# Optimization experiments

Measured on AMD Instinct MI355X. Metric: run time of the kernel, lower is better.

The kernel has to match this reference:

```python
import jax, jax.numpy as jnp
import numpy as np

L = 4096
E = 512   # embed dim
S = 1024  # state dim
H = 150   # Scorer hidden dim
GI = 2 * S + E
MAX_N = 10


def _scorer(x, W1, b1, W2, b2, W3, b3):
    h = jax.nn.relu(x @ W1 + b1)
    h = jax.nn.relu(h @ W2 + b2)
    return h @ W3 + b3  # [..., 1]


def setup_inputs() -> dict:
    key = jax.random.key(0)
    ks = jax.random.split(key, 16)
    def init(k, shape, fan_in):
        return jax.random.normal(k, shape, dtype=jnp.float32) / np.sqrt(fan_in)
    inp = {
        "embeds": jax.random.normal(ks[0], (L, E), dtype=jnp.float32),
        "states": jax.random.normal(ks[1], (L, S), dtype=jnp.float32),
        # attention Scorer params (input S)
        "aW1": init(ks[2], (S, H), S), "ab1": jnp.zeros((H,), jnp.float32),
        "aW2": init(ks[3], (H, H), H), "ab2": jnp.zeros((H,), jnp.float32),
        "aW3": init(ks[4], (H, 1), H), "ab3": jnp.zeros((1,), jnp.float32),
        # sm Scorer params (input GI)
        "sW1": init(ks[5], (GI, H), GI), "sb1": jnp.zeros((H,), jnp.float32),
        "sW2": init(ks[6], (H, H), H), "sb2": jnp.zeros((H,), jnp.float32),
        "sW3": init(ks[7], (H, 1), H), "sb3": jnp.zeros((1,), jnp.float32),
    }
    return inp


def reference(embeds, states, aW1, ab1, aW2, ab2, aW3, ab3,
              sW1, sb1, sW2, sb2, sW3, sb3):
    # per-token attention logits, computed once: [L]
    attns = _scorer(states, aW1, ab1, aW2, ab2, aW3, ab3)[:, 0]

    gs = []
    for n in range(1, MAX_N + 1):  # fixed small loop over window sizes
        M = L - n + 1                                  # number of windows
        starts = jnp.arange(M)
        idx = starts[:, None] + jnp.arange(n)          # [M, n] token indices
        w = jax.nn.softmax(attns[idx], axis=1)         # windowed softmax [M, n]
        pooled = jnp.einsum('mn,mne->me', w, embeds[idx])  # [M, E]
        g = jnp.concatenate([states[starts], states[starts + n - 1], pooled],
                            axis=1)                    # [M, 2S+E]
        gs.append(g)
    x = jnp.concatenate(gs, axis=0)                    # [T, GI], T = 10L-45
    scores = _scorer(x, sW1, sb1, sW2, sb2, sW3, sb3)[:, 0]  # [T]
    return scores
```

## Files before the change

kernel.cpp:

```cpp
#include <hip/hip_runtime.h>
#include <hip/hip_bf16.h>
#include <math.h>

#define LTOK 4096
#define EDIM 512
#define SDIM 1024
#define HDIM 150
#define PPAD 152
#define MAXN 10
#define TOTAL_ROWS 40915
#define KA 1536
#define NC 640
#define K2 160
#define NKT (KA / 32)

typedef _Float16 hfrag __attribute__((ext_vector_type(8)));
typedef float ffrag __attribute__((ext_vector_type(4)));


#define ITEMS_A   (LTOK * (KA / 8))
#define ITEMS_W   (NC * (KA / 8))
#define ITEMS_W2  (K2 * (K2 / 8))
#define ITEMS_A2  (K2 * (K2 / 8))
#define ITEMS_Z   (LTOK * K2 / 8)
#define ITEMS_TOT (ITEMS_A + ITEMS_W + ITEMS_W2 + ITEMS_A2 + ITEMS_Z)

__global__ __launch_bounds__(256) void prep_kernel(
    const float* __restrict__ embeds, const float* __restrict__ states,
    const float* __restrict__ aW1, const float* __restrict__ aW2,
    const float* __restrict__ sW1, const float* __restrict__ sW2,
    _Float16* __restrict__ Apk, _Float16* __restrict__ Wpk,
    _Float16* __restrict__ W2pk, _Float16* __restrict__ A2pk,
    _Float16* __restrict__ AH1h)
{
    int it = blockIdx.x * 256 + threadIdx.x;
    if (it < ITEMS_A) {
        const int rem = it % 3072;
        const int g = it / 3072, kt = rem >> 6, lane = rem & 63;
        const int row = g * 16 + (lane & 15);
        const int k0 = kt * 32 + (lane >> 4) * 8;
        const float* src = (k0 < SDIM) ? (states + (size_t)row * SDIM + k0)
                                       : (embeds + (size_t)row * EDIM + (k0 - SDIM));
        const float4 v0 = *(const float4*)src;
        const float4 v1 = *(const float4*)(src + 4);
        _Float16 o[8] = {(_Float16)v0.x, (_Float16)v0.y, (_Float16)v0.z, (_Float16)v0.w,
                         (_Float16)v1.x, (_Float16)v1.y, (_Float16)v1.z, (_Float16)v1.w};
        *(uint4*)(Apk + (size_t)it * 8) = *(uint4*)o;
        return;
    }
    it -= ITEMS_A;
    if (it < ITEMS_W) {
        const int rem = it % 3072;
        const int cg = it / 3072, kt = rem >> 6, lane = rem & 63;
        const int col = cg * 16 + (lane & 15);
        const int k0 = kt * 32 + (lane >> 4) * 8;
        const int g4 = (col < 600) ? (col / HDIM) : -1;
        const int cj = col % HDIM;
        _Float16 o[8];
        for (int j = 0; j < 8; ++j) {
            const int k = k0 + j;
            float wv = 0.f;
            if (g4 == 0 && k < SDIM) wv = sW1[(size_t)k * HDIM + cj];
            else if (g4 == 1 && k < SDIM) wv = sW1[(size_t)(SDIM + k) * HDIM + cj];
            else if (g4 == 2 && k < SDIM) wv = aW1[(size_t)k * HDIM + cj];
            else if (g4 == 3 && k >= SDIM) wv = sW1[(size_t)(SDIM + k) * HDIM + cj];
            o[j] = (_Float16)wv;
        }
        const size_t tk = (size_t)cg * 48 + kt;
        *(uint4*)(Wpk + (tk * 64 + lane) * 8) = *(uint4*)o;
        return;
    }
    it -= ITEMS_W;
    if (it < ITEMS_W2 + ITEMS_A2) {
        const bool is_a = (it >= ITEMS_W2);
        const int li = is_a ? (it - ITEMS_W2) : it;
        const float* src = is_a ? aW2 : sW2;
        _Float16* dst = is_a ? A2pk : W2pk;
        const int tk = li >> 6, lane = li & 63;
        const int col = (tk / 5) * 16 + (lane & 15);
        const int k0 = (tk % 5) * 32 + (lane >> 4) * 8;
        _Float16 o[8];
        for (int j = 0; j < 8; ++j) {
            const int k = k0 + j;
            float wv = (col < HDIM && k < HDIM) ? src[(size_t)k * HDIM + col] : 0.f;
            o[j] = (_Float16)wv;
        }
        *(uint4*)(dst + ((size_t)tk * 64 + lane) * 8) = *(uint4*)o;
        return;
    }
    it -= ITEMS_W2 + ITEMS_A2;
    if (it < ITEMS_Z) {
        const uint4 z = {0u, 0u, 0u, 0u};
        *(uint4*)(AH1h + (size_t)it * 8) = z;
    }
}

__global__ __launch_bounds__(256) void k_proj(
    const _Float16* __restrict__ Apk, const _Float16* __restrict__ Wpk,
    const float* __restrict__ ab1,
    float* __restrict__ P1, float* __restrict__ P2,
    float* __restrict__ PE, _Float16* __restrict__ AH1h)
{
    const int bM = blockIdx.x & 63, bN = blockIdx.x >> 6;
    const int tid = threadIdx.x;
    const int w = tid >> 6, lane = tid & 63;
    const int quad = lane >> 4, l16 = lane & 15;
    const int wm = w & 1, wn = w >> 1;

    const int gbase = bM * 4 + wm * 2;
    const int cgbase = bN * 4 + wn * 2;

    ffrag acc[2][2];
#pragma unroll
    for (int t = 0; t < 2; ++t)
#pragma unroll
        for (int u = 0; u < 2; ++u) acc[t][u] = (ffrag){0.f, 0.f, 0.f, 0.f};

    const _Float16* a0p = Apk + ((size_t)(gbase + 0) * NKT) * 512 + lane * 8;
    const _Float16* a1p = Apk + ((size_t)(gbase + 1) * NKT) * 512 + lane * 8;
    const _Float16* b0p = Wpk + ((size_t)(cgbase + 0) * NKT) * 512 + lane * 8;
    const _Float16* b1p = Wpk + ((size_t)(cgbase + 1) * NKT) * 512 + lane * 8;

#pragma unroll 4
    for (int kt = 0; kt < NKT; ++kt) {
        const hfrag a0 = *(const hfrag*)(a0p + (size_t)kt * 512);
        const hfrag a1 = *(const hfrag*)(a1p + (size_t)kt * 512);
        const hfrag b0 = *(const hfrag*)(b0p + (size_t)kt * 512);
        const hfrag b1 = *(const hfrag*)(b1p + (size_t)kt * 512);
        acc[0][0] = __builtin_amdgcn_mfma_f32_16x16x32_f16(a0, b0, acc[0][0], 0, 0, 0);
        acc[1][0] = __builtin_amdgcn_mfma_f32_16x16x32_f16(a1, b0, acc[1][0], 0, 0, 0);
        acc[0][1] = __builtin_amdgcn_mfma_f32_16x16x32_f16(a0, b1, acc[0][1], 0, 0, 0);
        acc[1][1] = __builtin_amdgcn_mfma_f32_16x16x32_f16(a1, b1, acc[1][1], 0, 0, 0);
    }

#pragma unroll
    for (int t = 0; t < 2; ++t)
#pragma unroll
        for (int u = 0; u < 2; ++u) {
            const int col = (cgbase + u) * 16 + l16;
#pragma unroll
            for (int r = 0; r < 4; ++r) {
                const int row = (gbase + t) * 16 + quad * 4 + r;
                const float v = acc[t][u][r];
                if (col < 150)      P1[(size_t)row * PPAD + col] = v;
                else if (col < 300) P2[(size_t)row * PPAD + (col - 150)] = v;
                else if (col < 450) AH1h[(size_t)row * K2 + (col - 300)] =
                                        (_Float16)fmaxf(v + ab1[col - 300], 0.f);
                else if (col < 600) PE[(size_t)row * PPAD + (col - 450)] = v;
            }
        }
}

__global__ __launch_bounds__(64) void attn_tail(
    const _Float16* __restrict__ AH1h, const _Float16* __restrict__ A2pk,
    const float* __restrict__ ab2, const float* __restrict__ aW3,
    const float* __restrict__ ab3, float* __restrict__ attns)
{
    const int tok0 = blockIdx.x * 16;
    const int lane = threadIdx.x;
    const int quad = lane >> 4, l16 = lane & 15;

    hfrag af[5];
#pragma unroll
    for (int ks = 0; ks < 5; ++ks)
        af[ks] = *(const hfrag*)(AH1h + (size_t)(tok0 + l16) * K2 + ks * 32 + quad * 8);

    float part[4] = {0.f, 0.f, 0.f, 0.f};
    for (int ct = 0; ct < 10; ++ct) {
        ffrag acc = (ffrag){0.f, 0.f, 0.f, 0.f};
#pragma unroll
        for (int ks = 0; ks < 5; ++ks) {
            const size_t tk = (size_t)ct * 5 + ks;
            const hfrag fb = *(const hfrag*)(A2pk + (tk * 64 + lane) * 8);
            acc = __builtin_amdgcn_mfma_f32_16x16x32_f16(af[ks], fb, acc, 0, 0, 0);
        }
        const int col = ct * 16 + l16;
        const float s2 = (col < HDIM) ? ab2[col] : 0.f;
        const float s3 = (col < HDIM) ? aW3[col] : 0.f;
#pragma unroll
        for (int r = 0; r < 4; ++r) part[r] += fmaxf(acc[r] + s2, 0.f) * s3;
    }

#pragma unroll
    for (int off = 1; off < 16; off <<= 1) {
#pragma unroll
        for (int r = 0; r < 4; ++r) part[r] += __shfl_xor(part[r], off, 64);
    }
    if (l16 == 0) {
        const float b3 = ab3[0];
#pragma unroll
        for (int r = 0; r < 4; ++r)
            attns[tok0 + quad * 4 + r] = part[r] + b3;
    }
}

#define RB2 64
__global__ __launch_bounds__(256) void span_kernel(
    const float* __restrict__ attns, const float* __restrict__ P1,
    const float* __restrict__ P2, const float* __restrict__ PE,
    const float* __restrict__ sb1, const _Float16* __restrict__ W2pk,
    const float* __restrict__ sb2, const float* __restrict__ sW3,
    const float* __restrict__ sb3, float* __restrict__ out)
{
    const int nIdx = blockIdx.x >> 6, mChunk = blockIdx.x & 63;
    const int n = nIdx + 1;
    const int Mn = LTOK - n + 1;
    const int m0 = mChunk * 64;
    const int nrows = min(64, Mn - m0);
    const int offn = nIdx * LTOK - (nIdx * (nIdx - 1)) / 2;

    const int tid = threadIdx.x;
    const int w = tid >> 6, lane = tid & 63, quad = lane >> 4, l16 = lane & 15;

    __shared__ __align__(16) _Float16 h1h[RB2 * K2];
    __shared__ float wgt[RB2][MAXN];

    if (tid < RB2) {
        const int m = min(m0 + tid, Mn - 1);
        float mx = -1e30f;
        for (int j = 0; j < n; ++j) mx = fmaxf(mx, attns[m + j]);
        float tp[MAXN]; float s = 0.f;
        for (int j = 0; j < n; ++j) { tp[j] = expf(attns[m + j] - mx); s += tp[j]; }
        const float inv = 1.f / s;
#pragma unroll
        for (int j = 0; j < MAXN; ++j) wgt[tid][j] = (j < n) ? tp[j] * inv : 0.f;
    }
    __syncthreads();

    for (int item = tid; item < RB2 * (K2 / 4); item += 256) {
        const int r = item / (K2 / 4), cq = item % (K2 / 4);
        const int c0 = cq * 4;
        const int m = min(m0 + r, Mn - 1);
        float4 a = {0.f, 0.f, 0.f, 0.f};
        if (c0 < HDIM) {
            const float4 p1 = *(const float4*)(P1 + (size_t)m * PPAD + c0);
            const float4 p2 = *(const float4*)(P2 + (size_t)(m + n - 1) * PPAD + c0);
            a.x = p1.x + p2.x; a.y = p1.y + p2.y;
            a.z = p1.z + p2.z; a.w = p1.w + p2.w;
#pragma unroll
            for (int j = 0; j < MAXN; ++j) {
                const int mj = min(m + j, LTOK - 1);
                const float4 pe = *(const float4*)(PE + (size_t)mj * PPAD + c0);
                const float wj = wgt[r][j];
                a.x = fmaf(wj, pe.x, a.x); a.y = fmaf(wj, pe.y, a.y);
                a.z = fmaf(wj, pe.z, a.z); a.w = fmaf(wj, pe.w, a.w);
            }
        }
        _Float16 o[4];
        o[0] = (c0 + 0 < HDIM) ? (_Float16)fmaxf(a.x + sb1[c0 + 0], 0.f) : (_Float16)0.f;
        o[1] = (c0 + 1 < HDIM) ? (_Float16)fmaxf(a.y + sb1[c0 + 1], 0.f) : (_Float16)0.f;
        o[2] = (c0 + 2 < HDIM) ? (_Float16)fmaxf(a.z + sb1[c0 + 2], 0.f) : (_Float16)0.f;
        o[3] = (c0 + 3 < HDIM) ? (_Float16)fmaxf(a.w + sb1[c0 + 3], 0.f) : (_Float16)0.f;
        *(uint2*)&h1h[r * K2 + c0] = *(uint2*)o;
    }
    __syncthreads();

    hfrag af[5];
#pragma unroll
    for (int ks = 0; ks < 5; ++ks)
        af[ks] = *(const hfrag*)&h1h[(w * 16 + l16) * K2 + ks * 32 + quad * 8];

    float part[4] = {0.f, 0.f, 0.f, 0.f};
    for (int ct = 0; ct < 10; ++ct) {
        ffrag acc = (ffrag){0.f, 0.f, 0.f, 0.f};
#pragma unroll
        for (int ks = 0; ks < 5; ++ks) {
            const size_t tk = (size_t)ct * 5 + ks;
            const hfrag fb = *(const hfrag*)(W2pk + (tk * 64 + lane) * 8);
            acc = __builtin_amdgcn_mfma_f32_16x16x32_f16(af[ks], fb, acc, 0, 0, 0);
        }
        const int col = ct * 16 + l16;
        const float s2 = (col < HDIM) ? sb2[col] : 0.f;
        const float s3 = (col < HDIM) ? sW3[col] : 0.f;
#pragma unroll
        for (int r = 0; r < 4; ++r) part[r] += fmaxf(acc[r] + s2, 0.f) * s3;
    }

#pragma unroll
    for (int off = 1; off < 16; off <<= 1) {
#pragma unroll
        for (int r = 0; r < 4; ++r) part[r] += __shfl_xor(part[r], off, 64);
    }
    if (l16 == 0) {
        const float b3 = sb3[0];
#pragma unroll
        for (int r = 0; r < 4; ++r) {
            const int lr = w * 16 + quad * 4 + r;
            if (lr < nrows) out[offn + m0 + lr] = part[r] + b3;
        }
    }
}

extern "C" void kernel_launch(void* const* d_in, const int* in_sizes, int n_in,
                              void* d_out, int out_size, void* d_ws, size_t ws_size,
                              hipStream_t stream) {
    const float* embeds = (const float*)d_in[0];
    const float* states = (const float*)d_in[1];
    const float* aW1 = (const float*)d_in[2];
    const float* ab1 = (const float*)d_in[3];
    const float* aW2 = (const float*)d_in[4];
    const float* ab2 = (const float*)d_in[5];
    const float* aW3 = (const float*)d_in[6];
    const float* ab3 = (const float*)d_in[7];
    const float* sW1 = (const float*)d_in[8];
    const float* sb1 = (const float*)d_in[9];
    const float* sW2 = (const float*)d_in[10];
    const float* sb2 = (const float*)d_in[11];
    const float* sW3 = (const float*)d_in[12];
    const float* sb3 = (const float*)d_in[13];
    float* out = (float*)d_out;

    float* attns = (float*)d_ws;
    float* P1 = attns + LTOK;
    float* P2 = P1 + (size_t)LTOK * PPAD;
    float* PE = P2 + (size_t)LTOK * PPAD;
    _Float16* AH1h = (_Float16*)(PE + (size_t)LTOK * PPAD);
    _Float16* Apk  = AH1h + (size_t)LTOK * K2;
    _Float16* Wpk  = Apk + (size_t)ITEMS_A * 8;
    _Float16* W2pk = Wpk + (size_t)NC * KA;
    _Float16* A2pk = W2pk + (size_t)K2 * K2;

    prep_kernel<<<(ITEMS_TOT + 255) / 256, 256, 0, stream>>>(
        embeds, states, aW1, aW2, sW1, sW2, Apk, Wpk, W2pk, A2pk, AH1h);
    k_proj<<<640, 256, 0, stream>>>(
        Apk, Wpk, ab1, P1, P2, PE, AH1h);
    attn_tail<<<LTOK / 16, 64, 0, stream>>>(
        AH1h, A2pk, ab2, aW3, ab3, attns);
    span_kernel<<<640, 256, 0, stream>>>(
        attns, P1, P2, PE, sb1, W2pk, sb2, sW3, sb3, out);
}
```

Before: 159.6 us.

## Fuse four kernels into one persistent kernel with grid-wide barriers

Merges the prep, projection GEMM, attention tail and span scorer kernels into a single persistent kernel sized to occupancy, separated by atomic-counter grid barriers. The goal is to remove three launch gaps and their tail drain. The attention tail now splits its column tiles across four waves and reduces partial sums in shared memory. The cost is a memset launch, barrier spin overhead, lower occupancy from launch bounds of three blocks, and a deadlock risk if not all blocks are co-resident.

```diff
diff --git a/kernel.cpp b/kernel.cpp
--- a/kernel.cpp
+++ b/kernel.cpp
@@ -1,5 +1,4 @@
 #include <hip/hip_runtime.h>
-#include <hip/hip_bf16.h>
 #include <math.h>
 
 #define LTOK 4096
@@ -13,6 +12,7 @@
 #define NC 640
 #define K2 160
 #define NKT (KA / 32)
+#define MAXGRID 640
 
 typedef _Float16 hfrag __attribute__((ext_vector_type(8)));
 typedef float ffrag __attribute__((ext_vector_type(4)));
@@ -25,7 +25,31 @@
 #define ITEMS_Z   (LTOK * K2 / 8)
 #define ITEMS_TOT (ITEMS_A + ITEMS_W + ITEMS_W2 + ITEMS_A2 + ITEMS_Z)
 
-__global__ __launch_bounds__(256) void prep_kernel(
+__device__ __forceinline__ void grid_barrier(int* bar) {
+    __syncthreads();
+    if (threadIdx.x == 0) {
+        __threadfence();
+        const int g = __hip_atomic_load(&bar[1], __ATOMIC_ACQUIRE,
+                                        __HIP_MEMORY_SCOPE_AGENT);
+        const int nb = (int)gridDim.x;
+        const int t = __hip_atomic_fetch_add(&bar[0], 1, __ATOMIC_ACQ_REL,
+                                             __HIP_MEMORY_SCOPE_AGENT);
+        if (t == nb - 1) {
+            __hip_atomic_store(&bar[0], 0, __ATOMIC_RELAXED,
+                               __HIP_MEMORY_SCOPE_AGENT);
+            __hip_atomic_fetch_add(&bar[1], 1, __ATOMIC_RELEASE,
+                                   __HIP_MEMORY_SCOPE_AGENT);
+        } else {
+            while (__hip_atomic_load(&bar[1], __ATOMIC_ACQUIRE,
+                                     __HIP_MEMORY_SCOPE_AGENT) == g) { }
+        }
+        __threadfence();
+    }
+    __syncthreads();
+}
+
+__device__ __forceinline__ void prep_item(
+    int it,
     const float* __restrict__ embeds, const float* __restrict__ states,
     const float* __restrict__ aW1, const float* __restrict__ aW2,
     const float* __restrict__ sW1, const float* __restrict__ sW2,
@@ -33,7 +57,6 @@
     _Float16* __restrict__ W2pk, _Float16* __restrict__ A2pk,
     _Float16* __restrict__ AH1h)
 {
-    int it = blockIdx.x * 256 + threadIdx.x;
     if (it < ITEMS_A) {
         const int rem = it % 3072;
         const int g = it / 3072, kt = rem >> 6, lane = rem & 63;
@@ -51,8 +74,8 @@
     it -= ITEMS_A;
     if (it < ITEMS_W) {
         const int rem = it % 3072;
-        const int cg = it / 3072, kt = rem >> 6, lane = rem & 63;
-        const int col = cg * 16 + (lane & 15);
+        const int cgi = it / 3072, kt = rem >> 6, lane = rem & 63;
+        const int col = cgi * 16 + (lane & 15);
         const int k0 = kt * 32 + (lane >> 4) * 8;
         const int g4 = (col < 600) ? (col / HDIM) : -1;
         const int cj = col % HDIM;
@@ -66,7 +89,7 @@
             else if (g4 == 3 && k >= SDIM) wv = sW1[(size_t)(SDIM + k) * HDIM + cj];
             o[j] = (_Float16)wv;
         }
-        const size_t tk = (size_t)cg * 48 + kt;
+        const size_t tk = (size_t)cgi * 48 + kt;
         *(uint4*)(Wpk + (tk * 64 + lane) * 8) = *(uint4*)o;
         return;
     }
@@ -95,198 +118,206 @@
     }
 }
 
-__global__ __launch_bounds__(256) void k_proj(
-    const _Float16* __restrict__ Apk, const _Float16* __restrict__ Wpk,
-    const float* __restrict__ ab1,
-    float* __restrict__ P1, float* __restrict__ P2,
-    float* __restrict__ PE, _Float16* __restrict__ AH1h)
+#define RB2 64
+__global__ __launch_bounds__(256, 3) void fused_all(
+    const float* __restrict__ embeds, const float* __restrict__ states,
+    const float* __restrict__ aW1, const float* __restrict__ ab1,
+    const float* __restrict__ aW2, const float* __restrict__ ab2,
+    const float* __restrict__ aW3, const float* __restrict__ ab3,
+    const float* __restrict__ sW1, const float* __restrict__ sb1,
+    const float* __restrict__ sW2, const float* __restrict__ sb2,
+    const float* __restrict__ sW3, const float* __restrict__ sb3,
+    float* __restrict__ out,
+    _Float16* __restrict__ Apk, _Float16* __restrict__ Wpk,
+    _Float16* __restrict__ W2pk, _Float16* __restrict__ A2pk,
+    _Float16* __restrict__ AH1h, float* __restrict__ attns,
+    float* __restrict__ P1, float* __restrict__ P2, float* __restrict__ PE,
+    int* __restrict__ bar)
 {
-    const int bM = blockIdx.x & 63, bN = blockIdx.x >> 6;
+    const int bid = blockIdx.x;
     const int tid = threadIdx.x;
     const int w = tid >> 6, lane = tid & 63;
     const int quad = lane >> 4, l16 = lane & 15;
-    const int wm = w & 1, wn = w >> 1;
-
-    const int gbase = bM * 4 + wm * 2;
-    const int cgbase = bN * 4 + wn * 2;
-
-    ffrag acc[2][2];
-#pragma unroll
-    for (int t = 0; t < 2; ++t)
-#pragma unroll
-        for (int u = 0; u < 2; ++u) acc[t][u] = (ffrag){0.f, 0.f, 0.f, 0.f};
-
-    const _Float16* a0p = Apk + ((size_t)(gbase + 0) * NKT) * 512 + lane * 8;
-    const _Float16* a1p = Apk + ((size_t)(gbase + 1) * NKT) * 512 + lane * 8;
-    const _Float16* b0p = Wpk + ((size_t)(cgbase + 0) * NKT) * 512 + lane * 8;
-    const _Float16* b1p = Wpk + ((size_t)(cgbase + 1) * NKT) * 512 + lane * 8;
+
+    __shared__ __align__(16) char smem[RB2 * K2 * 2 + RB2 * MAXN * 4];
+
+    for (int it = bid * 256 + tid; it < ITEMS_TOT; it += gridDim.x * 256)
+        prep_item(it, embeds, states, aW1, aW2, sW1, sW2,
+                  Apk, Wpk, W2pk, A2pk, AH1h);
+    grid_barrier(bar);
+
+    for (int tile = bid; tile < 640; tile += gridDim.x) {
+        const int bM = tile & 63, bN = tile >> 6;
+        const int wm = w & 1, wn = w >> 1;
+        const int gbase = bM * 4 + wm * 2;
+        const int cgbase = bN * 4 + wn * 2;
+
+        ffrag acc[2][2];
+#pragma unroll
+        for (int t = 0; t < 2; ++t)
+#pragma unroll
+            for (int u = 0; u < 2; ++u) acc[t][u] = (ffrag){0.f, 0.f, 0.f, 0.f};
+
+        const _Float16* a0p = Apk + ((size_t)(gbase + 0) * NKT) * 512 + lane * 8;
+        const _Float16* a1p = Apk + ((size_t)(gbase + 1) * NKT) * 512 + lane * 8;
+        const _Float16* b0p = Wpk + ((size_t)(cgbase + 0) * NKT) * 512 + lane * 8;
+        const _Float16* b1p = Wpk + ((size_t)(cgbase + 1) * NKT) * 512 + lane * 8;
 
 #pragma unroll 4
-    for (int kt = 0; kt < NKT; ++kt) {
-        const hfrag a0 = *(const hfrag*)(a0p + (size_t)kt * 512);
-        const hfrag a1 = *(const hfrag*)(a1p + (size_t)kt * 512);
-        const hfrag b0 = *(const hfrag*)(b0p + (size_t)kt * 512);
-        const hfrag b1 = *(const hfrag*)(b1p + (size_t)kt * 512);
-        acc[0][0] = __builtin_amdgcn_mfma_f32_16x16x32_f16(a0, b0, acc[0][0], 0, 0, 0);
-        acc[1][0] = __builtin_amdgcn_mfma_f32_16x16x32_f16(a1, b0, acc[1][0], 0, 0, 0);
-        acc[0][1] = __builtin_amdgcn_mfma_f32_16x16x32_f16(a0, b1, acc[0][1], 0, 0, 0);
-        acc[1][1] = __builtin_amdgcn_mfma_f32_16x16x32_f16(a1, b1, acc[1][1], 0, 0, 0);
-    }
-
-#pragma unroll
-    for (int t = 0; t < 2; ++t)
-#pragma unroll
-        for (int u = 0; u < 2; ++u) {
-            const int col = (cgbase + u) * 16 + l16;
+        for (int kt = 0; kt < NKT; ++kt) {
+            const hfrag a0 = *(const hfrag*)(a0p + (size_t)kt * 512);
+            const hfrag a1 = *(const hfrag*)(a1p + (size_t)kt * 512);
+            const hfrag b0 = *(const hfrag*)(b0p + (size_t)kt * 512);
+            const hfrag b1 = *(const hfrag*)(b1p + (size_t)kt * 512);
+            acc[0][0] = __builtin_amdgcn_mfma_f32_16x16x32_f16(a0, b0, acc[0][0], 0, 0, 0);
+            acc[1][0] = __builtin_amdgcn_mfma_f32_16x16x32_f16(a1, b0, acc[1][0], 0, 0, 0);
+            acc[0][1] = __builtin_amdgcn_mfma_f32_16x16x32_f16(a0, b1, acc[0][1], 0, 0, 0);
+            acc[1][1] = __builtin_amdgcn_mfma_f32_16x16x32_f16(a1, b1, acc[1][1], 0, 0, 0);
+        }
+
+#pragma unroll
+        for (int t = 0; t < 2; ++t)
+#pragma unroll
+            for (int u = 0; u < 2; ++u) {
+                const int col = (cgbase + u) * 16 + l16;
+#pragma unroll
+                for (int r = 0; r < 4; ++r) {
+                    const int row = (gbase + t) * 16 + quad * 4 + r;
+                    const float v = acc[t][u][r];
+                    if (col < 150)      P1[(size_t)row * PPAD + col] = v;
+                    else if (col < 300) P2[(size_t)row * PPAD + (col - 150)] = v;
+                    else if (col < 450) AH1h[(size_t)row * K2 + (col - 300)] =
+                                            (_Float16)fmaxf(v + ab1[col - 300], 0.f);
+                    else if (col < 600) PE[(size_t)row * PPAD + (col - 450)] = v;
+                }
+            }
+    }
+    grid_barrier(bar);
+
+    for (int tb = bid; tb < 256; tb += gridDim.x) {
+        const int tok0 = tb * 16;
+        hfrag af[5];
+#pragma unroll
+        for (int ks = 0; ks < 5; ++ks)
+            af[ks] = *(const hfrag*)(AH1h + (size_t)(tok0 + l16) * K2 + ks * 32 + quad * 8);
+
+        float part[4] = {0.f, 0.f, 0.f, 0.f};
+        for (int ct = w; ct < 10; ct += 4) {
+            ffrag acc = (ffrag){0.f, 0.f, 0.f, 0.f};
+#pragma unroll
+            for (int ks = 0; ks < 5; ++ks) {
+                const size_t tk = (size_t)ct * 5 + ks;
+                const hfrag fb = *(const hfrag*)(A2pk + (tk * 64 + lane) * 8);
+                acc = __builtin_amdgcn_mfma_f32_16x16x32_f16(af[ks], fb, acc, 0, 0, 0);
+            }
+            const int col = ct * 16 + l16;
+            const float s2 = (col < HDIM) ? ab2[col] : 0.f;
+            const float s3 = (col < HDIM) ? aW3[col] : 0.f;
+#pragma unroll
+            for (int r = 0; r < 4; ++r) part[r] += fmaxf(acc[r] + s2, 0.f) * s3;
+        }
+#pragma unroll
+        for (int off = 1; off < 16; off <<= 1) {
+#pragma unroll
+            for (int r = 0; r < 4; ++r) part[r] += __shfl_xor(part[r], off, 64);
+        }
+        float* red = (float*)smem;
+        if (l16 == 0) {
+#pragma unroll
+            for (int r = 0; r < 4; ++r) red[w * 16 + quad * 4 + r] = part[r];
+        }
+        __syncthreads();
+        if (tid < 16)
+            attns[tok0 + tid] = red[tid] + red[16 + tid] + red[32 + tid] +
+                                red[48 + tid] + ab3[0];
+        __syncthreads();
+    }
+    grid_barrier(bar);
+
+    for (int tile = bid; tile < 640; tile += gridDim.x) {
+        const int nIdx = tile >> 6, mChunk = tile & 63;
+        const int n = nIdx + 1;
+        const int Mn = LTOK - n + 1;
+        const int m0 = mChunk * 64;
+        const int nrows = min(64, Mn - m0);
+        const int offn = nIdx * LTOK - (nIdx * (nIdx - 1)) / 2;
+
+        _Float16* h1h = (_Float16*)smem;
+        float (*wgt)[MAXN] = (float(*)[MAXN])(smem + RB2 * K2 * 2);
+
+        __syncthreads();
+        if (tid < RB2) {
+            const int m = min(m0 + tid, Mn - 1);
+            float mx = -1e30f;
+            for (int j = 0; j < n; ++j) mx = fmaxf(mx, attns[m + j]);
+            float tp[MAXN]; float s = 0.f;
+            for (int j = 0; j < n; ++j) { tp[j] = expf(attns[m + j] - mx); s += tp[j]; }
+            const float inv = 1.f / s;
+#pragma unroll
+            for (int j = 0; j < MAXN; ++j) wgt[tid][j] = (j < n) ? tp[j] * inv : 0.f;
+        }
+        __syncthreads();
+
+        for (int item = tid; item < RB2 * (K2 / 4); item += 256) {
+            const int r = item / (K2 / 4), cq = item % (K2 / 4);
+            const int c0 = cq * 4;
+            const int m = min(m0 + r, Mn - 1);
+            float4 a = {0.f, 0.f, 0.f, 0.f};
+            if (c0 < HDIM) {
+                const float4 p1 = *(const float4*)(P1 + (size_t)m * PPAD + c0);
+                const float4 p2 = *(const float4*)(P2 + (size_t)(m + n - 1) * PPAD + c0);
+                a.x = p1.x + p2.x; a.y = p1.y + p2.y;
+                a.z = p1.z + p2.z; a.w = p1.w + p2.w;
+#pragma unroll
+                for (int j = 0; j < MAXN; ++j) {
+                    const int mj = min(m + j, LTOK - 1);
+                    const float4 pe = *(const float4*)(PE + (size_t)mj * PPAD + c0);
+                    const float wj = wgt[r][j];
+                    a.x = fmaf(wj, pe.x, a.x); a.y = fmaf(wj, pe.y, a.y);
+                    a.z = fmaf(wj, pe.z, a.z); a.w = fmaf(wj, pe.w, a.w);
+                }
+            }
+            _Float16 o[4];
+            o[0] = (c0 + 0 < HDIM) ? (_Float16)fmaxf(a.x + sb1[c0 + 0], 0.f) : (_Float16)0.f;
+            o[1] = (c0 + 1 < HDIM) ? (_Float16)fmaxf(a.y + sb1[c0 + 1], 0.f) : (_Float16)0.f;
+            o[2] = (c0 + 2 < HDIM) ? (_Float16)fmaxf(a.z + sb1[c0 + 2], 0.f) : (_Float16)0.f;
+            o[3] = (c0 + 3 < HDIM) ? (_Float16)fmaxf(a.w + sb1[c0 + 3], 0.f) : (_Float16)0.f;
+            *(uint2*)&h1h[r * K2 + c0] = *(uint2*)o;
+        }
+        __syncthreads();
+
+        hfrag af[5];
+#pragma unroll
+        for (int ks = 0; ks < 5; ++ks)
+            af[ks] = *(const hfrag*)&h1h[(w * 16 + l16) * K2 + ks * 32 + quad * 8];
+
+        float part[4] = {0.f, 0.f, 0.f, 0.f};
+        for (int ct = 0; ct < 10; ++ct) {
+            ffrag acc = (ffrag){0.f, 0.f, 0.f, 0.f};
+#pragma unroll
+            for (int ks = 0; ks < 5; ++ks) {
+                const size_t tk = (size_t)ct * 5 + ks;
+                const hfrag fb = *(const hfrag*)(W2pk + (tk * 64 + lane) * 8);
+                acc = __builtin_amdgcn_mfma_f32_16x16x32_f16(af[ks], fb, acc, 0, 0, 0);
+            }
+            const int col = ct * 16 + l16;
+            const float s2 = (col < HDIM) ? sb2[col] : 0.f;
+            const float s3 = (col < HDIM) ? sW3[col] : 0.f;
+#pragma unroll
+            for (int r = 0; r < 4; ++r) part[r] += fmaxf(acc[r] + s2, 0.f) * s3;
+        }
+#pragma unroll
+        for (int off = 1; off < 16; off <<= 1) {
+#pragma unroll
+            for (int r = 0; r < 4; ++r) part[r] += __shfl_xor(part[r], off, 64);
+        }
+        if (l16 == 0) {
+            const float b3 = sb3[0];
 #pragma unroll
             for (int r = 0; r < 4; ++r) {
-                const int row = (gbase + t) * 16 + quad * 4 + r;
-                const float v = acc[t][u][r];
-                if (col < 150)      P1[(size_t)row * PPAD + col] = v;
-                else if (col < 300) P2[(size_t)row * PPAD + (col - 150)] = v;
-                else if (col < 450) AH1h[(size_t)row * K2 + (col - 300)] =
-                                        (_Float16)fmaxf(v + ab1[col - 300], 0.f);
-                else if (col < 600) PE[(size_t)row * PPAD + (col - 450)] = v;
-            }
-        }
-}
-
-__global__ __launch_bounds__(64) void attn_tail(
-    const _Float16* __restrict__ AH1h, const _Float16* __restrict__ A2pk,
-    const float* __restrict__ ab2, const float* __restrict__ aW3,
-    const float* __restrict__ ab3, float* __restrict__ attns)
-{
-    const int tok0 = blockIdx.x * 16;
-    const int lane = threadIdx.x;
-    const int quad = lane >> 4, l16 = lane & 15;
-
-    hfrag af[5];
-#pragma unroll
-    for (int ks = 0; ks < 5; ++ks)
-        af[ks] = *(const hfrag*)(AH1h + (size_t)(tok0 + l16) * K2 + ks * 32 + quad * 8);
-
-    float part[4] = {0.f, 0.f, 0.f, 0.f};
-    for (int ct = 0; ct < 10; ++ct) {
-        ffrag acc = (ffrag){0.f, 0.f, 0.f, 0.f};
-#pragma unroll
-        for (int ks = 0; ks < 5; ++ks) {
-            const size_t tk = (size_t)ct * 5 + ks;
-            const hfrag fb = *(const hfrag*)(A2pk + (tk * 64 + lane) * 8);
-            acc = __builtin_amdgcn_mfma_f32_16x16x32_f16(af[ks], fb, acc, 0, 0, 0);
-        }
-        const int col = ct * 16 + l16;
-        const float s2 = (col < HDIM) ? ab2[col] : 0.f;
-        const float s3 = (col < HDIM) ? aW3[col] : 0.f;
-#pragma unroll
-        for (int r = 0; r < 4; ++r) part[r] += fmaxf(acc[r] + s2, 0.f) * s3;
-    }
-
-#pragma unroll
-    for (int off = 1; off < 16; off <<= 1) {
-#pragma unroll
-        for (int r = 0; r < 4; ++r) part[r] += __shfl_xor(part[r], off, 64);
-    }
-    if (l16 == 0) {
-        const float b3 = ab3[0];
-#pragma unroll
-        for (int r = 0; r < 4; ++r)
-            attns[tok0 + quad * 4 + r] = part[r] + b3;
-    }
-}
-
-#define RB2 64
-__global__ __launch_bounds__(256) void span_kernel(
-    const float* __restrict__ attns, const float* __restrict__ P1,
-    const float* __restrict__ P2, const float* __restrict__ PE,
-    const float* __restrict__ sb1, const _Float16* __restrict__ W2pk,
-    const float* __restrict__ sb2, const float* __restrict__ sW3,
-    const float* __restrict__ sb3, float* __restrict__ out)
-{
-    const int nIdx = blockIdx.x >> 6, mChunk = blockIdx.x & 63;
-    const int n = nIdx + 1;
-    const int Mn = LTOK - n + 1;
-    const int m0 = mChunk * 64;
-    const int nrows = min(64, Mn - m0);
-    const int offn = nIdx * LTOK - (nIdx * (nIdx - 1)) / 2;
-
-    const int tid = threadIdx.x;
-    const int w = tid >> 6, lane = tid & 63, quad = lane >> 4, l16 = lane & 15;
-
-    __shared__ __align__(16) _Float16 h1h[RB2 * K2];
-    __shared__ float wgt[RB2][MAXN];
-
-    if (tid < RB2) {
-        const int m = min(m0 + tid, Mn - 1);
-        float mx = -1e30f;
-        for (int j = 0; j < n; ++j) mx = fmaxf(mx, attns[m + j]);
-        float tp[MAXN]; float s = 0.f;
-        for (int j = 0; j < n; ++j) { tp[j] = expf(attns[m + j] - mx); s += tp[j]; }
-        const float inv = 1.f / s;
-#pragma unroll
-        for (int j = 0; j < MAXN; ++j) wgt[tid][j] = (j < n) ? tp[j] * inv : 0.f;
-    }
-    __syncthreads();
-
-    for (int item = tid; item < RB2 * (K2 / 4); item += 256) {
-        const int r = item / (K2 / 4), cq = item % (K2 / 4);
-        const int c0 = cq * 4;
-        const int m = min(m0 + r, Mn - 1);
-        float4 a = {0.f, 0.f, 0.f, 0.f};
-        if (c0 < HDIM) {
-            const float4 p1 = *(const float4*)(P1 + (size_t)m * PPAD + c0);
-            const float4 p2 = *(const float4*)(P2 + (size_t)(m + n - 1) * PPAD + c0);
-            a.x = p1.x + p2.x; a.y = p1.y + p2.y;
-            a.z = p1.z + p2.z; a.w = p1.w + p2.w;
-#pragma unroll
-            for (int j = 0; j < MAXN; ++j) {
-                const int mj = min(m + j, LTOK - 1);
-                const float4 pe = *(const float4*)(PE + (size_t)mj * PPAD + c0);
-                const float wj = wgt[r][j];
-                a.x = fmaf(wj, pe.x, a.x); a.y = fmaf(wj, pe.y, a.y);
-                a.z = fmaf(wj, pe.z, a.z); a.w = fmaf(wj, pe.w, a.w);
-            }
-        }
-        _Float16 o[4];
-        o[0] = (c0 + 0 < HDIM) ? (_Float16)fmaxf(a.x + sb1[c0 + 0], 0.f) : (_Float16)0.f;
-        o[1] = (c0 + 1 < HDIM) ? (_Float16)fmaxf(a.y + sb1[c0 + 1], 0.f) : (_Float16)0.f;
-        o[2] = (c0 + 2 < HDIM) ? (_Float16)fmaxf(a.z + sb1[c0 + 2], 0.f) : (_Float16)0.f;
-        o[3] = (c0 + 3 < HDIM) ? (_Float16)fmaxf(a.w + sb1[c0 + 3], 0.f) : (_Float16)0.f;
-        *(uint2*)&h1h[r * K2 + c0] = *(uint2*)o;
-    }
-    __syncthreads();
-
-    hfrag af[5];
-#pragma unroll
-    for (int ks = 0; ks < 5; ++ks)
-        af[ks] = *(const hfrag*)&h1h[(w * 16 + l16) * K2 + ks * 32 + quad * 8];
-
-    float part[4] = {0.f, 0.f, 0.f, 0.f};
-    for (int ct = 0; ct < 10; ++ct) {
-        ffrag acc = (ffrag){0.f, 0.f, 0.f, 0.f};
-#pragma unroll
-        for (int ks = 0; ks < 5; ++ks) {
-            const size_t tk = (size_t)ct * 5 + ks;
-            const hfrag fb = *(const hfrag*)(W2pk + (tk * 64 + lane) * 8);
-            acc = __builtin_amdgcn_mfma_f32_16x16x32_f16(af[ks], fb, acc, 0, 0, 0);
-        }
-        const int col = ct * 16 + l16;
-        const float s2 = (col < HDIM) ? sb2[col] : 0.f;
-        const float s3 = (col < HDIM) ? sW3[col] : 0.f;
-#pragma unroll
-        for (int r = 0; r < 4; ++r) part[r] += fmaxf(acc[r] + s2, 0.f) * s3;
-    }
-
-#pragma unroll
-    for (int off = 1; off < 16; off <<= 1) {
-#pragma unroll
-        for (int r = 0; r < 4; ++r) part[r] += __shfl_xor(part[r], off, 64);
-    }
-    if (l16 == 0) {
-        const float b3 = sb3[0];
-#pragma unroll
-        for (int r = 0; r < 4; ++r) {
-            const int lr = w * 16 + quad * 4 + r;
-            if (lr < nrows) out[offn + m0 + lr] = part[r] + b3;
+                const int lr = w * 16 + quad * 4 + r;
+                if (lr < nrows) out[offn + m0 + lr] = part[r] + b3;
+            }
         }
     }
 }
@@ -319,13 +350,17 @@
     _Float16* Wpk  = Apk + (size_t)ITEMS_A * 8;
     _Float16* W2pk = Wpk + (size_t)NC * KA;
     _Float16* A2pk = W2pk + (size_t)K2 * K2;
-
-    prep_kernel<<<(ITEMS_TOT + 255) / 256, 256, 0, stream>>>(
-        embeds, states, aW1, aW2, sW1, sW2, Apk, Wpk, W2pk, A2pk, AH1h);
-    k_proj<<<640, 256, 0, stream>>>(
-        Apk, Wpk, ab1, P1, P2, PE, AH1h);
-    attn_tail<<<LTOK / 16, 64, 0, stream>>>(
-        AH1h, A2pk, ab2, aW3, ab3, attns);
-    span_kernel<<<640, 256, 0, stream>>>(
-        attns, P1, P2, PE, sb1, W2pk, sb2, sW3, sb3, out);
+    int* bar = (int*)(A2pk + (size_t)K2 * K2);
+
+    int maxB = 0;
+    (void)hipOccupancyMaxActiveBlocksPerMultiprocessor(&maxB, fused_all, 256, 0);
+    if (maxB < 1) maxB = 1;
+    int grid = 256 * maxB;
+    if (grid > MAXGRID) grid = MAXGRID;
+
+    hipMemsetAsync(bar, 0, 2 * sizeof(int), stream);
+    fused_all<<<grid, 256, 0, stream>>>(
+        embeds, states, aW1, ab1, aW2, ab2, aW3, ab3, sW1, sb1,
+        sW2, sb2, sW3, sb3, out,
+        Apk, Wpk, W2pk, A2pk, AH1h, attns, P1, P2, PE, bar);
 }
```

New measurement: 360.8 us. 126% more time.

## Fuse attention scorer tail into projection kernel and store projections in fp16

Applied to the files above, without the earlier changes.

Moves the attention-scorer second layer into k_proj: the first 64 blocks compute the attention hidden layer for 64 tokens, keep it in shared memory and finish the logits there. This removes the separate attn_tail launch and the global AH1h round trip. The remaining projection tiles use 160-aligned segments and loop only over the K range that has nonzero weights (states or embeds half), which cuts wasted MFMA work. P1/P2/PE are now stored as fp16, halving the traffic read by span_kernel at some cost in precision. The attention blocks do a long serial K loop with 10 accumulators and may become a tail on the critical path.

```diff
diff --git a/kernel.cpp b/kernel.cpp
--- a/kernel.cpp
+++ b/kernel.cpp
@@ -1,42 +1,40 @@
 #include <hip/hip_runtime.h>
-#include <hip/hip_bf16.h>
 #include <math.h>
 
 #define LTOK 4096
 #define EDIM 512
 #define SDIM 1024
 #define HDIM 150
-#define PPAD 152
+#define SEG 160
 #define MAXN 10
 #define TOTAL_ROWS 40915
 #define KA 1536
-#define NC 640
+#define NKT 48
 #define K2 160
-#define NKT (KA / 32)
+#define NCG 42
 
 typedef _Float16 hfrag __attribute__((ext_vector_type(8)));
+typedef _Float16 h4 __attribute__((ext_vector_type(4)));
 typedef float ffrag __attribute__((ext_vector_type(4)));
 
 
 #define ITEMS_A   (LTOK * (KA / 8))
-#define ITEMS_W   (NC * (KA / 8))
+#define ITEMS_W   (NCG * NKT * 64)
 #define ITEMS_W2  (K2 * (K2 / 8))
 #define ITEMS_A2  (K2 * (K2 / 8))
-#define ITEMS_Z   (LTOK * K2 / 8)
-#define ITEMS_TOT (ITEMS_A + ITEMS_W + ITEMS_W2 + ITEMS_A2 + ITEMS_Z)
+#define ITEMS_TOT (ITEMS_A + ITEMS_W + ITEMS_W2 + ITEMS_A2)
 
 __global__ __launch_bounds__(256) void prep_kernel(
     const float* __restrict__ embeds, const float* __restrict__ states,
     const float* __restrict__ aW1, const float* __restrict__ aW2,
     const float* __restrict__ sW1, const float* __restrict__ sW2,
     _Float16* __restrict__ Apk, _Float16* __restrict__ Wpk,
-    _Float16* __restrict__ W2pk, _Float16* __restrict__ A2pk,
-    _Float16* __restrict__ AH1h)
+    _Float16* __restrict__ W2pk, _Float16* __restrict__ A2pk)
 {
     int it = blockIdx.x * 256 + threadIdx.x;
     if (it < ITEMS_A) {
-        const int rem = it % 3072;
-        const int g = it / 3072, kt = rem >> 6, lane = rem & 63;
+        const int rem = it % (NKT * 64);
+        const int g = it / (NKT * 64), kt = rem >> 6, lane = rem & 63;
         const int row = g * 16 + (lane & 15);
         const int k0 = kt * 32 + (lane >> 4) * 8;
         const float* src = (k0 < SDIM) ? (states + (size_t)row * SDIM + k0)
@@ -50,24 +48,29 @@
     }
     it -= ITEMS_A;
     if (it < ITEMS_W) {
-        const int rem = it % 3072;
-        const int cg = it / 3072, kt = rem >> 6, lane = rem & 63;
-        const int col = cg * 16 + (lane & 15);
+        const int rem = it % (NKT * 64);
+        const int cgi = it / (NKT * 64), kt = rem >> 6, lane = rem & 63;
+        const int col = cgi * 16 + (lane & 15);
         const int k0 = kt * 32 + (lane >> 4) * 8;
-        const int g4 = (col < 600) ? (col / HDIM) : -1;
-        const int cj = col % HDIM;
         _Float16 o[8];
         for (int j = 0; j < 8; ++j) {
             const int k = k0 + j;
             float wv = 0.f;
-            if (g4 == 0 && k < SDIM) wv = sW1[(size_t)k * HDIM + cj];
-            else if (g4 == 1 && k < SDIM) wv = sW1[(size_t)(SDIM + k) * HDIM + cj];
-            else if (g4 == 2 && k < SDIM) wv = aW1[(size_t)k * HDIM + cj];
-            else if (g4 == 3 && k >= SDIM) wv = sW1[(size_t)(SDIM + k) * HDIM + cj];
+            if (col < 160) {
+                if (col < HDIM && k < SDIM) wv = sW1[(size_t)k * HDIM + col];
+            } else if (col < 320) {
+                const int cj = col - 160;
+                if (cj < HDIM && k < SDIM) wv = sW1[(size_t)(SDIM + k) * HDIM + cj];
+            } else if (col < 480) {
+                const int cj = col - 320;
+                if (cj < HDIM && k >= SDIM) wv = sW1[(size_t)(SDIM + k) * HDIM + cj];
+            } else if (col >= 512) {
+                const int cj = col - 512;
+                if (cj < HDIM && k < SDIM) wv = aW1[(size_t)k * HDIM + cj];
+            }
             o[j] = (_Float16)wv;
         }
-        const size_t tk = (size_t)cg * 48 + kt;
-        *(uint4*)(Wpk + (tk * 64 + lane) * 8) = *(uint4*)o;
+        *(uint4*)(Wpk + ((size_t)((size_t)cgi * NKT + kt) * 64 + lane) * 8) = *(uint4*)o;
         return;
     }
     it -= ITEMS_W;
@@ -86,29 +89,95 @@
             o[j] = (_Float16)wv;
         }
         *(uint4*)(dst + ((size_t)tk * 64 + lane) * 8) = *(uint4*)o;
-        return;
-    }
-    it -= ITEMS_W2 + ITEMS_A2;
-    if (it < ITEMS_Z) {
-        const uint4 z = {0u, 0u, 0u, 0u};
-        *(uint4*)(AH1h + (size_t)it * 8) = z;
     }
 }
 
 __global__ __launch_bounds__(256) void k_proj(
     const _Float16* __restrict__ Apk, const _Float16* __restrict__ Wpk,
-    const float* __restrict__ ab1,
-    float* __restrict__ P1, float* __restrict__ P2,
-    float* __restrict__ PE, _Float16* __restrict__ AH1h)
+    const _Float16* __restrict__ A2pk,
+    const float* __restrict__ ab1, const float* __restrict__ ab2,
+    const float* __restrict__ aW3, const float* __restrict__ ab3,
+    _Float16* __restrict__ P1h, _Float16* __restrict__ P2h,
+    _Float16* __restrict__ PEh, float* __restrict__ attns)
 {
-    const int bM = blockIdx.x & 63, bN = blockIdx.x >> 6;
+    const int bid = blockIdx.x;
     const int tid = threadIdx.x;
     const int w = tid >> 6, lane = tid & 63;
     const int quad = lane >> 4, l16 = lane & 15;
+
+    __shared__ __align__(16) _Float16 ah1[64 * SEG];
+
+    if (bid < 64) {
+        const int tok0 = bid * 64;
+        const int g = tok0 / 16 + w;
+
+        ffrag acc[10];
+#pragma unroll
+        for (int c = 0; c < 10; ++c) acc[c] = (ffrag){0.f, 0.f, 0.f, 0.f};
+
+        const _Float16* ap = Apk + ((size_t)g * NKT) * 512 + lane * 8;
+        for (int kt = 0; kt < 32; ++kt) {
+            const hfrag a = *(const hfrag*)(ap + (size_t)kt * 512);
+#pragma unroll
+            for (int c = 0; c < 10; ++c) {
+                const hfrag b = *(const hfrag*)(
+                    Wpk + (((size_t)(32 + c) * NKT + kt) * 64 + lane) * 8);
+                acc[c] = __builtin_amdgcn_mfma_f32_16x16x32_f16(a, b, acc[c], 0, 0, 0);
+            }
+        }
+#pragma unroll
+        for (int c = 0; c < 10; ++c) {
+            const int col = c * 16 + l16;
+            const float b1 = (col < HDIM) ? ab1[col] : 0.f;
+#pragma unroll
+            for (int r = 0; r < 4; ++r) {
+                const int row = w * 16 + quad * 4 + r;
+                ah1[row * SEG + col] = (_Float16)fmaxf(acc[c][r] + b1, 0.f);
+            }
+        }
+        __syncthreads();
+
+        hfrag af[5];
+#pragma unroll
+        for (int ks = 0; ks < 5; ++ks)
+            af[ks] = *(const hfrag*)&ah1[(w * 16 + l16) * SEG + ks * 32 + quad * 8];
+
+        float part[4] = {0.f, 0.f, 0.f, 0.f};
+        for (int ct = 0; ct < 10; ++ct) {
+            ffrag a2 = (ffrag){0.f, 0.f, 0.f, 0.f};
+#pragma unroll
+            for (int ks = 0; ks < 5; ++ks) {
+                const hfrag fb = *(const hfrag*)(
+                    A2pk + ((size_t)(ct * 5 + ks) * 64 + lane) * 8);
+                a2 = __builtin_amdgcn_mfma_f32_16x16x32_f16(af[ks], fb, a2, 0, 0, 0);
+            }
+            const int col = ct * 16 + l16;
+            const float s2 = (col < HDIM) ? ab2[col] : 0.f;
+            const float s3 = (col < HDIM) ? aW3[col] : 0.f;
+#pragma unroll
+            for (int r = 0; r < 4; ++r) part[r] += fmaxf(a2[r] + s2, 0.f) * s3;
+        }
+#pragma unroll
+        for (int off = 1; off < 16; off <<= 1) {
+#pragma unroll
+            for (int r = 0; r < 4; ++r) part[r] += __shfl_xor(part[r], off, 64);
+        }
+        if (l16 == 0) {
+            const float b3 = ab3[0];
+#pragma unroll
+            for (int r = 0; r < 4; ++r)
+                attns[tok0 + w * 16 + quad * 4 + r] = part[r] + b3;
+        }
+        return;
+    }
+
+    const int tile = bid - 64;
+    const int bM = tile & 63, bN = tile >> 6;
     const int wm = w & 1, wn = w >> 1;
-
     const int gbase = bM * 4 + wm * 2;
     const int cgbase = bN * 4 + wn * 2;
+    const int kt0 = (bN >= 5) ? 32 : 0;
+    const int kt1 = (bN >= 5) ? 48 : 32;
 
     ffrag acc[2][2];
 #pragma unroll
@@ -122,7 +191,7 @@
     const _Float16* b1p = Wpk + ((size_t)(cgbase + 1) * NKT) * 512 + lane * 8;
 
 #pragma unroll 4
-    for (int kt = 0; kt < NKT; ++kt) {
+    for (int kt = kt0; kt < kt1; ++kt) {
         const hfrag a0 = *(const hfrag*)(a0p + (size_t)kt * 512);
         const hfrag a1 = *(const hfrag*)(a1p + (size_t)kt * 512);
         const hfrag b0 = *(const hfrag*)(b0p + (size_t)kt * 512);
@@ -141,63 +210,18 @@
 #pragma unroll
             for (int r = 0; r < 4; ++r) {
                 const int row = (gbase + t) * 16 + quad * 4 + r;
-                const float v = acc[t][u][r];
-                if (col < 150)      P1[(size_t)row * PPAD + col] = v;
-                else if (col < 300) P2[(size_t)row * PPAD + (col - 150)] = v;
-                else if (col < 450) AH1h[(size_t)row * K2 + (col - 300)] =
-                                        (_Float16)fmaxf(v + ab1[col - 300], 0.f);
-                else if (col < 600) PE[(size_t)row * PPAD + (col - 450)] = v;
-            }
-        }
-}
-
-__global__ __launch_bounds__(64) void attn_tail(
-    const _Float16* __restrict__ AH1h, const _Float16* __restrict__ A2pk,
-    const float* __restrict__ ab2, const float* __restrict__ aW3,
-    const float* __restrict__ ab3, float* __restrict__ attns)
-{
-    const int tok0 = blockIdx.x * 16;
-    const int lane = threadIdx.x;
-    const int quad = lane >> 4, l16 = lane & 15;
-
-    hfrag af[5];
-#pragma unroll
-    for (int ks = 0; ks < 5; ++ks)
-        af[ks] = *(const hfrag*)(AH1h + (size_t)(tok0 + l16) * K2 + ks * 32 + quad * 8);
-
-    float part[4] = {0.f, 0.f, 0.f, 0.f};
-    for (int ct = 0; ct < 10; ++ct) {
-        ffrag acc = (ffrag){0.f, 0.f, 0.f, 0.f};
-#pragma unroll
-        for (int ks = 0; ks < 5; ++ks) {
-            const size_t tk = (size_t)ct * 5 + ks;
-            const hfrag fb = *(const hfrag*)(A2pk + (tk * 64 + lane) * 8);
-            acc = __builtin_amdgcn_mfma_f32_16x16x32_f16(af[ks], fb, acc, 0, 0, 0);
-        }
-        const int col = ct * 16 + l16;
-        const float s2 = (col < HDIM) ? ab2[col] : 0.f;
-        const float s3 = (col < HDIM) ? aW3[col] : 0.f;
-#pragma unroll
-        for (int r = 0; r < 4; ++r) part[r] += fmaxf(acc[r] + s2, 0.f) * s3;
-    }
-
-#pragma unroll
-    for (int off = 1; off < 16; off <<= 1) {
-#pragma unroll
-        for (int r = 0; r < 4; ++r) part[r] += __shfl_xor(part[r], off, 64);
-    }
-    if (l16 == 0) {
-        const float b3 = ab3[0];
-#pragma unroll
-        for (int r = 0; r < 4; ++r)
-            attns[tok0 + quad * 4 + r] = part[r] + b3;
-    }
+                const _Float16 hv = (_Float16)acc[t][u][r];
+                if (col < 160)      P1h[(size_t)row * SEG + col] = hv;
+                else if (col < 320) P2h[(size_t)row * SEG + (col - 160)] = hv;
+                else if (col < 480) PEh[(size_t)row * SEG + (col - 320)] = hv;
+            }
+        }
 }
 
 #define RB2 64
 __global__ __launch_bounds__(256) void span_kernel(
-    const float* __restrict__ attns, const float* __restrict__ P1,
-    const float* __restrict__ P2, const float* __restrict__ PE,
+    const float* __restrict__ attns, const _Float16* __restrict__ P1h,
+    const _Float16* __restrict__ P2h, const _Float16* __restrict__ PEh,
     const float* __restrict__ sb1, const _Float16* __restrict__ W2pk,
     const float* __restrict__ sb2, const float* __restrict__ sW3,
     const float* __restrict__ sb3, float* __restrict__ out)
@@ -233,17 +257,21 @@
         const int m = min(m0 + r, Mn - 1);
         float4 a = {0.f, 0.f, 0.f, 0.f};
         if (c0 < HDIM) {
-            const float4 p1 = *(const float4*)(P1 + (size_t)m * PPAD + c0);
-            const float4 p2 = *(const float4*)(P2 + (size_t)(m + n - 1) * PPAD + c0);
-            a.x = p1.x + p2.x; a.y = p1.y + p2.y;
-            a.z = p1.z + p2.z; a.w = p1.w + p2.w;
+            const h4 p1 = *(const h4*)(P1h + (size_t)m * SEG + c0);
+            const h4 p2 = *(const h4*)(P2h + (size_t)(m + n - 1) * SEG + c0);
+            a.x = (float)p1[0] + (float)p2[0];
+            a.y = (float)p1[1] + (float)p2[1];
+            a.z = (float)p1[2] + (float)p2[2];
+            a.w = (float)p1[3] + (float)p2[3];
 #pragma unroll
             for (int j = 0; j < MAXN; ++j) {
                 const int mj = min(m + j, LTOK - 1);
-                const float4 pe = *(const float4*)(PE + (size_t)mj * PPAD + c0);
+                const h4 pe = *(const h4*)(PEh + (size_t)mj * SEG + c0);
                 const float wj = wgt[r][j];
-                a.x = fmaf(wj, pe.x, a.x); a.y = fmaf(wj, pe.y, a.y);
-                a.z = fmaf(wj, pe.z, a.z); a.w = fmaf(wj, pe.w, a.w);
+                a.x = fmaf(wj, (float)pe[0], a.x);
+                a.y = fmaf(wj, (float)pe[1], a.y);
+                a.z = fmaf(wj, (float)pe[2], a.z);
+                a.w = fmaf(wj, (float)pe[3], a.w);
             }
         }
         _Float16 o[4];
@@ -265,8 +293,8 @@
         ffrag acc = (ffrag){0.f, 0.f, 0.f, 0.f};
 #pragma unroll
         for (int ks = 0; ks < 5; ++ks) {
-            const size_t tk = (size_t)ct * 5 + ks;
-            const hfrag fb = *(const hfrag*)(W2pk + (tk * 64 + lane) * 8);
+            const hfrag fb = *(const hfrag*)(
+                W2pk + ((size_t)(ct * 5 + ks) * 64 + lane) * 8);
             acc = __builtin_amdgcn_mfma_f32_16x16x32_f16(af[ks], fb, acc, 0, 0, 0);
         }
         const int col = ct * 16 + l16;
@@ -311,21 +339,18 @@
     float* out = (float*)d_out;
 
     float* attns = (float*)d_ws;
-    float* P1 = attns + LTOK;
-    float* P2 = P1 + (size_t)LTOK * PPAD;
-    float* PE = P2 + (size_t)LTOK * PPAD;
-    _Float16* AH1h = (_Float16*)(PE + (size_t)LTOK * PPAD);
-    _Float16* Apk  = AH1h + (size_t)LTOK * K2;
+    _Float16* P1h  = (_Float16*)(attns + LTOK);
+    _Float16* P2h  = P1h + (size_t)LTOK * SEG;
+    _Float16* PEh  = P2h + (size_t)LTOK * SEG;
+    _Float16* Apk  = PEh + (size_t)LTOK * SEG;
     _Float16* Wpk  = Apk + (size_t)ITEMS_A * 8;
-    _Float16* W2pk = Wpk + (size_t)NC * KA;
-    _Float16* A2pk = W2pk + (size_t)K2 * K2;
-
-    prep_kernel<<<(ITEMS_TOT + 255) / 256, 256, 0, stream>>>(
-        embeds, states, aW1, aW2, sW1, sW2, Apk, Wpk, W2pk, A2pk, AH1h);
-    k_proj<<<640, 256, 0, stream>>>(
-        Apk, Wpk, ab1, P1, P2, PE, AH1h);
-    attn_tail<<<LTOK / 16, 64, 0, stream>>>(
-        AH1h, A2pk, ab2, aW3, ab3, attns);
+    _Float16* W2pk = Wpk + (size_t)ITEMS_W * 8;
+    _Float16* A2pk = W2pk + (size_t)ITEMS_W2 * 8;
+
+    prep_kernel<<<ITEMS_TOT / 256, 256, 0, stream>>>(
+        embeds, states, aW1, aW2, sW1, sW2, Apk, Wpk, W2pk, A2pk);
+    k_proj<<<576, 256, 0, stream>>>(
+        Apk, Wpk, A2pk, ab1, ab2, aW3, ab3, P1h, P2h, PEh, attns);
     span_kernel<<<640, 256, 0, stream>>>(
-        attns, P1, P2, PE, sb1, W2pk, sb2, sW3, sb3, out);
+        attns, P1h, P2h, PEh, sb1, W2pk, sb2, sW3, sb3, out);
 }
```

New measurement: 155.9 us. 1.02x faster.
